# Kernel tuning notes

Hardware: AMD Instinct MI355X
Metric: run time of the kernel (lower is better)

## Reference

```python
import jax, jax.numpy as jnp
import numpy as np

# ---- config derived from init_kwargs (level=3, max_levels=14, max_size=256,
# max_channels=512, margin=10, start_cutoff=2, critical_layers=2, window_size=6) ----
SCALE_FACTOR = 2          # size_prev(16) < size(32)
UP_FACTOR = 2 * SCALE_FACTOR   # 4
UP_PAD = (13, 10)         # p = 24 - 2*sf = 20 -> ((p+1)//2 + 2*sf - 1, p//2)
DOWN_PAD = (5, 5)         # p = 12 - 2 = 10 -> ((p+1)//2, p//2)
MARGIN = 10
CUTOFF, BAND_HALF = 5.656854249492381, 10.343145750507619   # level 3, sr=128
CUTOFF_PREV, BAND_HALF_PREV = 4.0, 4.0                      # level 2, sr=128
SR = 32 * SCALE_FACTOR * 2  # 128


def _lowpass_filter(n_taps, cutoff, band_half, sr):
    # Kaiser-windowed sinc lowpass, identical math to the torch module.
    df = 2 * band_half / (sr / 2)
    atten = 2.285 * (n_taps - 1) * np.pi * df + 7.95
    if atten > 50:
        beta = 0.1102 * (atten - 8.7)
    elif atten >= 21:
        beta = 0.5842 * (atten - 21) ** 0.4 + 0.07886 * (atten - 21)
    else:
        beta = 0.0
    ind = np.arange(n_taps) - (n_taps - 1) / 2
    window = np.i0(beta * np.sqrt(1 - (2 * ind / (n_taps - 1)) ** 2)) / np.i0(beta)
    return 2 * cutoff / sr * np.sinc(2 * cutoff / sr * ind) * window


def setup_inputs() -> dict:
    key = jax.random.key(0)
    x = jax.random.normal(key, (16, 512, 36, 36), dtype=jnp.float32)
    up = _lowpass_filter(24, CUTOFF_PREV, BAND_HALF_PREV, SR)
    up = up / up.sum() * 2 * SCALE_FACTOR
    down = _lowpass_filter(12, CUTOFF, BAND_HALF, SR)
    down = down / down.sum()
    return {
        "x": x,
        "up_filter": jnp.asarray(up, dtype=jnp.float32),
        "down_filter": jnp.asarray(down, dtype=jnp.float32),
    }


def _upfirdn1d(x, kernel, up, down, pad, axis):
    # Separable 1D upfirdn along axis (2=H, 3=W) of NCHW tensor.
    # Matches upfirdn2d_native: zero-insert upsample (up-1 trailing zeros),
    # pad, correlate with flipped kernel, stride-`down` decimate.
    # lhs_dilation inserts up-1 zeros BETWEEN samples; adding up-1 to the
    # right pad reproduces the trailing zeros of the native op exactly.
    B, C, H, W = x.shape
    k = kernel.shape[0]
    w = jnp.flip(kernel).astype(x.dtype)
    if axis == 3:
        rhs = w.reshape(1, 1, 1, k)
        lhs_dil, strides = (1, up), (1, down)
        padding = ((0, 0), (pad[0], pad[1] + up - 1))
    else:
        rhs = w.reshape(1, 1, k, 1)
        lhs_dil, strides = (up, 1), (down, 1)
        padding = ((pad[0], pad[1] + up - 1), (0, 0))
    y = jax.lax.conv_general_dilated(
        x.reshape(B * C, 1, H, W), rhs,
        window_strides=strides, padding=padding, lhs_dilation=lhs_dil,
        dimension_numbers=("NCHW", "OIHW", "NCHW"))
    return y.reshape(B, C, y.shape[2], y.shape[3])


def reference(x, up_filter, down_filter):
    # Upsample x4 (separable: width then height)
    x = _upfirdn1d(x, up_filter, UP_FACTOR, 1, UP_PAD, axis=3)
    x = _upfirdn1d(x, up_filter, UP_FACTOR, 1, UP_PAD, axis=2)   # (16,512,144,144)
    # Pointwise nonlinearity in the high-res domain (alias-free)
    x = jax.nn.leaky_relu(x, 0.2)
    # Downsample x2 (separable: width then height)
    x = _upfirdn1d(x, down_filter, 1, 2, DOWN_PAD, axis=3)
    x = _upfirdn1d(x, down_filter, 1, 2, DOWN_PAD, axis=2)       # (16,512,72,72)
    m = SCALE_FACTOR * MARGIN // 2  # 10
    return x[:, :, m:-m, m:-m]      # (16,512,52,52)
```

## Files before the change

kernel.cpp:

```cpp
#include <hip/hip_runtime.h>


typedef float v2f __attribute__((ext_vector_type(2)));

static __device__ __forceinline__ v2f vsplat(float s) { v2f v; v.x = s; v.y = s; return v; }
#define VFMA(A, S, C) __builtin_elementwise_fma((A), vsplat(S), (C))

#define SCATTER(J, hv)                                                        \
    _Pragma("unroll")                                                         \
    for (int k = (J) & 1; k <= 11; k += 2) {                                  \
        if ((J) - k >= 0 && (((J) - k) >> 1) < 26)                            \
            acc[((J) - k) >> 1] = VFMA(hv, dn[11 - k], acc[((J) - k) >> 1]);  \
    }

#define DO_J(J, A, B, C, D, E, F)                                             \
    do {                                                                      \
        const int q_ = ((J) + 1) & 3;                                         \
        v2f h_ = (A) * vsplat(up[20 + q_]);                                   \
        h_ = VFMA((B), up[16 + q_], h_);                                      \
        h_ = VFMA((C), up[12 + q_], h_);                                      \
        h_ = VFMA((D), up[8 + q_], h_);                                       \
        h_ = VFMA((E), up[4 + q_], h_);                                       \
        h_ = VFMA((F), up[q_], h_);                                           \
        h_ = __builtin_elementwise_max(h_, h_ * vsplat(0.2f));                \
        SCATTER(J, h_);                                                       \
    } while (0)

#define GROUP(G, T0, T1, T2, T3, T4, T5)                                      \
    do {                                                                      \
        T0 = wbase[(G) + 5];                                                  \
        DO_J(4 * (G) - 1, T1, T2, T3, T4, T5, T0);                            \
        DO_J(4 * (G), T1, T2, T3, T4, T5, T0);                                \
        DO_J(4 * (G) + 1, T1, T2, T3, T4, T5, T0);                            \
        DO_J(4 * (G) + 2, T1, T2, T3, T4, T5, T0);                            \
    } while (0)

#define GROUP_TAIL(T0, T1, T2, T3, T4, T5)                                    \
    do {                                                                      \
        T0 = wbase[20];                                                       \
        DO_J(59, T1, T2, T3, T4, T5, T0);                                     \
        DO_J(60, T1, T2, T3, T4, T5, T0);                                     \
        DO_J(61, T1, T2, T3, T4, T5, T0);                                     \
    } while (0)

#define P3LD(RA, RB, M)                                                       \
    RA = p3b[(M)*53];                                                         \
    RB = p3b[((M) + 1) * 53];

#define P3OUT(J, A, B, C, D, E, F, G, H, I, JJ, K, L)                         \
    do {                                                                      \
        v2f a_ = (A) * vsplat(dn[11]);                                        \
        a_ = VFMA((B), dn[10], a_);                                           \
        a_ = VFMA((C), dn[9], a_);                                            \
        a_ = VFMA((D), dn[8], a_);                                            \
        a_ = VFMA((E), dn[7], a_);                                            \
        a_ = VFMA((F), dn[6], a_);                                            \
        a_ = VFMA((G), dn[5], a_);                                            \
        a_ = VFMA((H), dn[4], a_);                                            \
        a_ = VFMA((I), dn[3], a_);                                            \
        a_ = VFMA((JJ), dn[2], a_);                                           \
        a_ = VFMA((K), dn[1], a_);                                            \
        a_ = VFMA((L), dn[0], a_);                                            \
        const int o_ = (13 * s + (J)) * 52 + ow;                              \
        op0[o_] = a_.x;                                                       \
        op1[o_] = a_.y;                                                       \
    } while (0)

__global__ __launch_bounds__(256, 3)
void afa_kernel(const float* __restrict__ x,
                const float* __restrict__ upf,
                const float* __restrict__ dnf,
                float* __restrict__ out)
{
    __shared__ v2f buf[114 * 53];

    const int tid = threadIdx.x;
    const size_t q0 = (size_t)blockIdx.x * 2;
    const float* __restrict__ xp0 = x + q0 * 1296;
    const float* __restrict__ xp1 = xp0 + 1296;
    float* __restrict__ op0 = out + q0 * 2704;
    float* __restrict__ op1 = op0 + 2704;

    float up[24];
#pragma unroll
    for (int i = 0; i < 24; ++i) up[i] = upf[i];
    float dn[12];
#pragma unroll
    for (int i = 0; i < 12; ++i) dn[i] = dnf[i];

    if (tid < 204) {
        const int s1 = tid / 34;
        const int mw = tid % 34 + 1;

        v2f xr[11];
#pragma unroll
        for (int jj = 0; jj < 11; ++jj) {
            int row = 5 * s1 + 1 + jj;
            row = row > 35 ? 35 : row;
            xr[jj].x = xp0[row * 36 + mw];
            xr[jj].y = xp1[row * 36 + mw];
        }
        const int lh0  = 20 * s1;
        const int jmax = (s1 == 5) ? 14 : 20;
#pragma unroll
        for (int j = 0; j < 20; ++j) {
            if (j < jmax) {
                const int rel = ((j + 5) >> 2) - 1;
                const int c0  = 20 + ((j + 1) & 3);
                v2f a = vsplat(0.f);
#pragma unroll
                for (int t = 0; t < 6; ++t)
                    a = VFMA(xr[rel + t], up[c0 - 4 * t], a);
                buf[(lh0 + j) * 35 + (mw - 1)] = a;
            }
        }
    }
    __syncthreads();

    const int  lh   = tid % 114;
    const int  p    = tid / 114;
    const bool act2 = tid < 228;
    v2f acc[26];
    if (act2) {
        const v2f* __restrict__ wbase = &buf[lh * 35 + 13 * p];
        v2f w0 = wbase[0], w1 = wbase[1], w2 = wbase[2],
            w3 = wbase[3], w4 = wbase[4], w5 = wbase[5];
#pragma unroll
        for (int o = 0; o < 26; ++o) acc[o] = vsplat(0.f);

        DO_J(0, w0, w1, w2, w3, w4, w5);
        DO_J(1, w0, w1, w2, w3, w4, w5);
        DO_J(2, w0, w1, w2, w3, w4, w5);
        GROUP(1,  w0, w1, w2, w3, w4, w5);
        GROUP(2,  w1, w2, w3, w4, w5, w0);
        GROUP(3,  w2, w3, w4, w5, w0, w1);
        GROUP(4,  w3, w4, w5, w0, w1, w2);
        GROUP(5,  w4, w5, w0, w1, w2, w3);
        GROUP(6,  w5, w0, w1, w2, w3, w4);
        GROUP(7,  w0, w1, w2, w3, w4, w5);
        GROUP(8,  w1, w2, w3, w4, w5, w0);
        GROUP(9,  w2, w3, w4, w5, w0, w1);
        GROUP(10, w3, w4, w5, w0, w1, w2);
        GROUP(11, w4, w5, w0, w1, w2, w3);
        GROUP(12, w5, w0, w1, w2, w3, w4);
        GROUP(13, w0, w1, w2, w3, w4, w5);
        GROUP(14, w1, w2, w3, w4, w5, w0);
        GROUP_TAIL(w2, w3, w4, w5, w0, w1);
    }
    __syncthreads();

    if (act2) {
        v2f* __restrict__ tw = &buf[lh * 53 + 26 * p];
#pragma unroll
        for (int o = 0; o < 26; ++o) tw[o] = acc[o];
    }
    __syncthreads();

    if (tid < 208) {
        const int ow = tid % 52;
        const int s  = tid / 52;
        const v2f* __restrict__ p3b = &buf[(26 * s) * 53 + ow];

        v2f r0, r1, r2, r3, r4, r5, r6, r7, r8, r9, r10, r11;
        P3LD(r0, r1, 0)  P3LD(r2, r3, 2)  P3LD(r4, r5, 4)
        P3LD(r6, r7, 6)  P3LD(r8, r9, 8)  P3LD(r10, r11, 10)

        P3OUT(0, r0, r1, r2, r3, r4, r5, r6, r7, r8, r9, r10, r11);
        P3LD(r0, r1, 12)
        P3OUT(1, r2, r3, r4, r5, r6, r7, r8, r9, r10, r11, r0, r1);
        P3LD(r2, r3, 14)
        P3OUT(2, r4, r5, r6, r7, r8, r9, r10, r11, r0, r1, r2, r3);
        P3LD(r4, r5, 16)
        P3OUT(3, r6, r7, r8, r9, r10, r11, r0, r1, r2, r3, r4, r5);
        P3LD(r6, r7, 18)
        P3OUT(4, r8, r9, r10, r11, r0, r1, r2, r3, r4, r5, r6, r7);
        P3LD(r8, r9, 20)
        P3OUT(5, r10, r11, r0, r1, r2, r3, r4, r5, r6, r7, r8, r9);
        P3LD(r10, r11, 22)
        P3OUT(6, r0, r1, r2, r3, r4, r5, r6, r7, r8, r9, r10, r11);
        P3LD(r0, r1, 24)
        P3OUT(7, r2, r3, r4, r5, r6, r7, r8, r9, r10, r11, r0, r1);
        P3LD(r2, r3, 26)
        P3OUT(8, r4, r5, r6, r7, r8, r9, r10, r11, r0, r1, r2, r3);
        P3LD(r4, r5, 28)
        P3OUT(9, r6, r7, r8, r9, r10, r11, r0, r1, r2, r3, r4, r5);
        P3LD(r6, r7, 30)
        P3OUT(10, r8, r9, r10, r11, r0, r1, r2, r3, r4, r5, r6, r7);
        P3LD(r8, r9, 32)
        P3OUT(11, r10, r11, r0, r1, r2, r3, r4, r5, r6, r7, r8, r9);
        P3LD(r10, r11, 34)
        P3OUT(12, r0, r1, r2, r3, r4, r5, r6, r7, r8, r9, r10, r11);
    }
}

extern "C" void kernel_launch(void* const* d_in, const int* in_sizes, int n_in,
                              void* d_out, int out_size, void* d_ws, size_t ws_size,
                              hipStream_t stream)
{
    const float* x  = (const float*)d_in[0];
    const float* up = (const float*)d_in[1];
    const float* dn = (const float*)d_in[2];
    float* out = (float*)d_out;

    const int pairs = 16 * 512 / 2;
    afa_kernel<<<dim3(pairs), dim3(256), 0, stream>>>(x, up, dn, out);
}
```

Baseline: 143.6 us.

## Process one channel per block with scalar floats instead of packed channel pairs

```diff
diff --git a/kernel.cpp b/kernel.cpp
--- a/kernel.cpp
+++ b/kernel.cpp
@@ -1,10 +1,7 @@
 #include <hip/hip_runtime.h>
 
 
-typedef float v2f __attribute__((ext_vector_type(2)));
-
-static __device__ __forceinline__ v2f vsplat(float s) { v2f v; v.x = s; v.y = s; return v; }
-#define VFMA(A, S, C) __builtin_elementwise_fma((A), vsplat(S), (C))
+#define VFMA(A, S, C) fmaf((A), (S), (C))
 
 #define SCATTER(J, hv)                                                        \
     _Pragma("unroll")                                                         \
@@ -16,13 +13,13 @@
 #define DO_J(J, A, B, C, D, E, F)                                             \
     do {                                                                      \
         const int q_ = ((J) + 1) & 3;                                         \
-        v2f h_ = (A) * vsplat(up[20 + q_]);                                   \
+        float h_ = (A) * up[20 + q_];                                         \
         h_ = VFMA((B), up[16 + q_], h_);                                      \
         h_ = VFMA((C), up[12 + q_], h_);                                      \
         h_ = VFMA((D), up[8 + q_], h_);                                       \
         h_ = VFMA((E), up[4 + q_], h_);                                       \
         h_ = VFMA((F), up[q_], h_);                                           \
-        h_ = __builtin_elementwise_max(h_, h_ * vsplat(0.2f));                \
+        h_ = fmaxf(h_, 0.2f * h_);                                            \
         SCATTER(J, h_);                                                       \
     } while (0)
 
@@ -49,7 +46,7 @@
 
 #define P3OUT(J, A, B, C, D, E, F, G, H, I, JJ, K, L)                         \
     do {                                                                      \
-        v2f a_ = (A) * vsplat(dn[11]);                                        \
+        float a_ = (A) * dn[11];                                              \
         a_ = VFMA((B), dn[10], a_);                                           \
         a_ = VFMA((C), dn[9], a_);                                            \
         a_ = VFMA((D), dn[8], a_);                                            \
@@ -61,25 +58,21 @@
         a_ = VFMA((JJ), dn[2], a_);                                           \
         a_ = VFMA((K), dn[1], a_);                                            \
         a_ = VFMA((L), dn[0], a_);                                            \
-        const int o_ = (13 * s + (J)) * 52 + ow;                              \
-        op0[o_] = a_.x;                                                       \
-        op1[o_] = a_.y;                                                       \
+        op0[(13 * s + (J)) * 52 + ow] = a_;                                   \
     } while (0)
 
-__global__ __launch_bounds__(256, 3)
+__global__ __launch_bounds__(256, 6)
 void afa_kernel(const float* __restrict__ x,
                 const float* __restrict__ upf,
                 const float* __restrict__ dnf,
                 float* __restrict__ out)
 {
-    __shared__ v2f buf[114 * 53];
+    __shared__ float buf[114 * 53];
 
     const int tid = threadIdx.x;
-    const size_t q0 = (size_t)blockIdx.x * 2;
+    const size_t q0 = (size_t)blockIdx.x;
     const float* __restrict__ xp0 = x + q0 * 1296;
-    const float* __restrict__ xp1 = xp0 + 1296;
     float* __restrict__ op0 = out + q0 * 2704;
-    float* __restrict__ op1 = op0 + 2704;
 
     float up[24];
 #pragma unroll
@@ -92,13 +85,12 @@
         const int s1 = tid / 34;
         const int mw = tid % 34 + 1;
 
-        v2f xr[11];
+        float xr[11];
 #pragma unroll
         for (int jj = 0; jj < 11; ++jj) {
             int row = 5 * s1 + 1 + jj;
             row = row > 35 ? 35 : row;
-            xr[jj].x = xp0[row * 36 + mw];
-            xr[jj].y = xp1[row * 36 + mw];
+            xr[jj] = xp0[row * 36 + mw];
         }
         const int lh0  = 20 * s1;
         const int jmax = (s1 == 5) ? 14 : 20;
@@ -107,7 +99,7 @@
             if (j < jmax) {
                 const int rel = ((j + 5) >> 2) - 1;
                 const int c0  = 20 + ((j + 1) & 3);
-                v2f a = vsplat(0.f);
+                float a = 0.f;
 #pragma unroll
                 for (int t = 0; t < 6; ++t)
                     a = VFMA(xr[rel + t], up[c0 - 4 * t], a);
@@ -120,13 +112,13 @@
     const int  lh   = tid % 114;
     const int  p    = tid / 114;
     const bool act2 = tid < 228;
-    v2f acc[26];
+    float acc[26];
     if (act2) {
-        const v2f* __restrict__ wbase = &buf[lh * 35 + 13 * p];
-        v2f w0 = wbase[0], w1 = wbase[1], w2 = wbase[2],
-            w3 = wbase[3], w4 = wbase[4], w5 = wbase[5];
+        const float* __restrict__ wbase = &buf[lh * 35 + 13 * p];
+        float w0 = wbase[0], w1 = wbase[1], w2 = wbase[2],
+              w3 = wbase[3], w4 = wbase[4], w5 = wbase[5];
 #pragma unroll
-        for (int o = 0; o < 26; ++o) acc[o] = vsplat(0.f);
+        for (int o = 0; o < 26; ++o) acc[o] = 0.f;
 
         DO_J(0, w0, w1, w2, w3, w4, w5);
         DO_J(1, w0, w1, w2, w3, w4, w5);
@@ -150,7 +142,7 @@
     __syncthreads();
 
     if (act2) {
-        v2f* __restrict__ tw = &buf[lh * 53 + 26 * p];
+        float* __restrict__ tw = &buf[lh * 53 + 26 * p];
 #pragma unroll
         for (int o = 0; o < 26; ++o) tw[o] = acc[o];
     }
@@ -159,9 +151,9 @@
     if (tid < 208) {
         const int ow = tid % 52;
         const int s  = tid / 52;
-        const v2f* __restrict__ p3b = &buf[(26 * s) * 53 + ow];
+        const float* __restrict__ p3b = &buf[(26 * s) * 53 + ow];
 
-        v2f r0, r1, r2, r3, r4, r5, r6, r7, r8, r9, r10, r11;
+        float r0, r1, r2, r3, r4, r5, r6, r7, r8, r9, r10, r11;
         P3LD(r0, r1, 0)  P3LD(r2, r3, 2)  P3LD(r4, r5, 4)
         P3LD(r6, r7, 6)  P3LD(r8, r9, 8)  P3LD(r10, r11, 10)
 
@@ -202,6 +194,5 @@
     const float* dn = (const float*)d_in[2];
     float* out = (float*)d_out;
 
-    const int pairs = 16 * 512 / 2;
-    afa_kernel<<<dim3(pairs), dim3(256), 0, stream>>>(x, up, dn, out);
+    afa_kernel<<<dim3(16 * 512), dim3(256), 0, stream>>>(x, up, dn, out);
 }
```

Result: slower. 151.4 us (+5.5%).

## Double block to 512 threads, splitting each stage's work into smaller per-thread chunks

Applied to the files above, without the earlier changes.

```diff
diff --git a/kernel.cpp b/kernel.cpp
--- a/kernel.cpp
+++ b/kernel.cpp
@@ -9,7 +9,7 @@
 #define SCATTER(J, hv)                                                        \
     _Pragma("unroll")                                                         \
     for (int k = (J) & 1; k <= 11; k += 2) {                                  \
-        if ((J) - k >= 0 && (((J) - k) >> 1) < 26)                            \
+        if ((J) - k >= 0 && (((J) - k) >> 1) < 14)                            \
             acc[((J) - k) >> 1] = VFMA(hv, dn[11 - k], acc[((J) - k) >> 1]);  \
     }
 
@@ -37,10 +37,10 @@
 
 #define GROUP_TAIL(T0, T1, T2, T3, T4, T5)                                    \
     do {                                                                      \
-        T0 = wbase[20];                                                       \
-        DO_J(59, T1, T2, T3, T4, T5, T0);                                     \
-        DO_J(60, T1, T2, T3, T4, T5, T0);                                     \
-        DO_J(61, T1, T2, T3, T4, T5, T0);                                     \
+        T0 = wbase[14];                                                       \
+        DO_J(35, T1, T2, T3, T4, T5, T0);                                     \
+        DO_J(36, T1, T2, T3, T4, T5, T0);                                     \
+        DO_J(37, T1, T2, T3, T4, T5, T0);                                     \
     } while (0)
 
 #define P3LD(RA, RB, M)                                                       \
@@ -61,18 +61,20 @@
         a_ = VFMA((JJ), dn[2], a_);                                           \
         a_ = VFMA((K), dn[1], a_);                                            \
         a_ = VFMA((L), dn[0], a_);                                            \
-        const int o_ = (13 * s + (J)) * 52 + ow;                              \
-        op0[o_] = a_.x;                                                       \
-        op1[o_] = a_.y;                                                       \
+        const int oh_ = 7 * s + (J);                                          \
+        if (oh_ < 52) {                                                       \
+            op0[oh_ * 52 + ow] = a_.x;                                        \
+            op1[oh_ * 52 + ow] = a_.y;                                        \
+        }                                                                     \
     } while (0)
 
-__global__ __launch_bounds__(256, 3)
+__global__ __launch_bounds__(512, 6)
 void afa_kernel(const float* __restrict__ x,
                 const float* __restrict__ upf,
                 const float* __restrict__ dnf,
                 float* __restrict__ out)
 {
-    __shared__ v2f buf[114 * 53];
+    __shared__ v2f buf[122 * 53];
 
     const int tid = threadIdx.x;
     const size_t q0 = (size_t)blockIdx.x * 2;
@@ -88,78 +90,76 @@
 #pragma unroll
     for (int i = 0; i < 12; ++i) dn[i] = dnf[i];
 
-    if (tid < 204) {
+    if (tid < 510) {
         const int s1 = tid / 34;
         const int mw = tid % 34 + 1;
 
-        v2f xr[11];
+        v2f xr[8];
 #pragma unroll
-        for (int jj = 0; jj < 11; ++jj) {
-            int row = 5 * s1 + 1 + jj;
+        for (int i = 0; i < 8; ++i) {
+            int row = 2 * s1 + 1 + i;
             row = row > 35 ? 35 : row;
-            xr[jj].x = xp0[row * 36 + mw];
-            xr[jj].y = xp1[row * 36 + mw];
+            xr[i].x = xp0[row * 36 + mw];
+            xr[i].y = xp1[row * 36 + mw];
         }
-        const int lh0  = 20 * s1;
-        const int jmax = (s1 == 5) ? 14 : 20;
 #pragma unroll
-        for (int j = 0; j < 20; ++j) {
-            if (j < jmax) {
-                const int rel = ((j + 5) >> 2) - 1;
-                const int c0  = 20 + ((j + 1) & 3);
-                v2f a = vsplat(0.f);
+        for (int j = 0; j < 8; ++j) {
+            const int rel = ((j + 5) >> 2) - 1;
+            const int c0  = 20 + ((j + 1) & 3);
+            v2f a = vsplat(0.f);
 #pragma unroll
-                for (int t = 0; t < 6; ++t)
-                    a = VFMA(xr[rel + t], up[c0 - 4 * t], a);
-                buf[(lh0 + j) * 35 + (mw - 1)] = a;
-            }
+            for (int t = 0; t < 6; ++t)
+                a = VFMA(xr[rel + t], up[c0 - 4 * t], a);
+            const int lh = 8 * s1 + j;
+            if (lh < 114)
+                buf[lh * 35 + (mw - 1)] = a;
         }
     }
     __syncthreads();
 
     const int  lh   = tid % 114;
     const int  p    = tid / 114;
-    const bool act2 = tid < 228;
-    v2f acc[26];
+    const bool act2 = tid < 456;
+    v2f acc[14];
     if (act2) {
-        const v2f* __restrict__ wbase = &buf[lh * 35 + 13 * p];
+        const int L0 = 26 * p - ((p & 1) << 1);
+        const v2f* __restrict__ wbase = &buf[lh * 35 + (L0 >> 2)];
         v2f w0 = wbase[0], w1 = wbase[1], w2 = wbase[2],
             w3 = wbase[3], w4 = wbase[4], w5 = wbase[5];
 #pragma unroll
-        for (int o = 0; o < 26; ++o) acc[o] = vsplat(0.f);
+        for (int o = 0; o < 14; ++o) acc[o] = vsplat(0.f);
 
         DO_J(0, w0, w1, w2, w3, w4, w5);
         DO_J(1, w0, w1, w2, w3, w4, w5);
         DO_J(2, w0, w1, w2, w3, w4, w5);
-        GROUP(1,  w0, w1, w2, w3, w4, w5);
-        GROUP(2,  w1, w2, w3, w4, w5, w0);
-        GROUP(3,  w2, w3, w4, w5, w0, w1);
-        GROUP(4,  w3, w4, w5, w0, w1, w2);
-        GROUP(5,  w4, w5, w0, w1, w2, w3);
-        GROUP(6,  w5, w0, w1, w2, w3, w4);
-        GROUP(7,  w0, w1, w2, w3, w4, w5);
-        GROUP(8,  w1, w2, w3, w4, w5, w0);
-        GROUP(9,  w2, w3, w4, w5, w0, w1);
-        GROUP(10, w3, w4, w5, w0, w1, w2);
-        GROUP(11, w4, w5, w0, w1, w2, w3);
-        GROUP(12, w5, w0, w1, w2, w3, w4);
-        GROUP(13, w0, w1, w2, w3, w4, w5);
-        GROUP(14, w1, w2, w3, w4, w5, w0);
+        GROUP(1, w0, w1, w2, w3, w4, w5);
+        GROUP(2, w1, w2, w3, w4, w5, w0);
+        GROUP(3, w2, w3, w4, w5, w0, w1);
+        GROUP(4, w3, w4, w5, w0, w1, w2);
+        GROUP(5, w4, w5, w0, w1, w2, w3);
+        GROUP(6, w5, w0, w1, w2, w3, w4);
+        GROUP(7, w0, w1, w2, w3, w4, w5);
+        GROUP(8, w1, w2, w3, w4, w5, w0);
         GROUP_TAIL(w2, w3, w4, w5, w0, w1);
     }
     __syncthreads();
 
     if (act2) {
-        v2f* __restrict__ tw = &buf[lh * 53 + 26 * p];
+        v2f* __restrict__ tw = &buf[lh * 53 + 13 * p];
+        if (p & 1) {
 #pragma unroll
-        for (int o = 0; o < 26; ++o) tw[o] = acc[o];
+            for (int oo = 0; oo < 13; ++oo) tw[oo] = acc[oo + 1];
+        } else {
+#pragma unroll
+            for (int oo = 0; oo < 13; ++oo) tw[oo] = acc[oo];
+        }
     }
     __syncthreads();
 
-    if (tid < 208) {
+    if (tid < 416) {
         const int ow = tid % 52;
         const int s  = tid / 52;
-        const v2f* __restrict__ p3b = &buf[(26 * s) * 53 + ow];
+        const v2f* __restrict__ p3b = &buf[(14 * s) * 53 + ow];
 
         v2f r0, r1, r2, r3, r4, r5, r6, r7, r8, r9, r10, r11;
         P3LD(r0, r1, 0)  P3LD(r2, r3, 2)  P3LD(r4, r5, 4)
@@ -178,18 +178,6 @@
         P3OUT(5, r10, r11, r0, r1, r2, r3, r4, r5, r6, r7, r8, r9);
         P3LD(r10, r11, 22)
         P3OUT(6, r0, r1, r2, r3, r4, r5, r6, r7, r8, r9, r10, r11);
-        P3LD(r0, r1, 24)
-        P3OUT(7, r2, r3, r4, r5, r6, r7, r8, r9, r10, r11, r0, r1);
-        P3LD(r2, r3, 26)
-        P3OUT(8, r4, r5, r6, r7, r8, r9, r10, r11, r0, r1, r2, r3);
-        P3LD(r4, r5, 28)
-        P3OUT(9, r6, r7, r8, r9, r10, r11, r0, r1, r2, r3, r4, r5);
-        P3LD(r6, r7, 30)
-        P3OUT(10, r8, r9, r10, r11, r0, r1, r2, r3, r4, r5, r6, r7);
-        P3LD(r8, r9, 32)
-        P3OUT(11, r10, r11, r0, r1, r2, r3, r4, r5, r6, r7, r8, r9);
-        P3LD(r10, r11, 34)
-        P3OUT(12, r0, r1, r2, r3, r4, r5, r6, r7, r8, r9, r10, r11);
     }
 }
 
@@ -203,5 +191,5 @@
     float* out = (float*)d_out;
 
     const int pairs = 16 * 512 / 2;
-    afa_kernel<<<dim3(pairs), dim3(256), 0, stream>>>(x, up, dn, out);
+    afa_kernel<<<dim3(pairs), dim3(512), 0, stream>>>(x, up, dn, out);
 }
```

Result: slower. 154.4 us (+7.5%).
